# Performance work log

Hardware: AMD Instinct MI355X
Metric: run time of the kernel (lower is better)

Reference implementation:

```python
import jax, jax.numpy as jnp
import numpy as np

N_IN, N_HID, N_OUT = 700, 512, 20
B, T = 256, 100
TAU, TAU_O, THR, GAMMA = 0.6, 0.6, 0.6, 0.3

# Triangle surrogate spike (TriangleCall): heaviside fwd, triangular pseudo-derivative bwd
@jax.custom_vjp
def _spike(v):
    return (v >= THR).astype(v.dtype)

def _spike_fwd(v):
    return _spike(v), v

def _spike_bwd(v, g):
    sg = GAMMA * jnp.maximum(0.0, 1.0 - jnp.abs((v - THR) / THR))
    return (g * sg,)

_spike.defvjp(_spike_fwd, _spike_bwd)


def setup_inputs():
    key = jax.random.key(0)
    k1, k2, k3, k4, k5 = jax.random.split(key, 5)
    # binary input / target spike trains
    x = (jax.random.uniform(k1, (B, T, N_IN)) < 0.2).astype(jnp.float32)
    label = (jax.random.uniform(k2, (B, T, N_OUT)) < 0.1).astype(jnp.float32)
    # analog tile weights: fc1 and out halved at init, recurrent ~ U[0,1)/sqrt(n_hidden)
    W_fc1 = jax.random.normal(k3, (N_HID, N_IN), jnp.float32) * 0.05
    W_rec = jax.random.uniform(k4, (N_HID, N_HID), jnp.float32) / np.float32(np.sqrt(N_HID))
    W_out = jax.random.normal(k5, (N_OUT, N_HID), jnp.float32) * 0.05
    return {'x': x, 'label': label, 'W_fc1': W_fc1, 'W_rec': W_rec, 'W_out': W_out}


def reference(x, label, W_fc1, W_rec, W_out):
    b = x.shape[0]
    z = lambda n: jnp.zeros((b, n), x.dtype)
    carry0 = (z(N_HID), z(N_HID), z(N_OUT), z(N_OUT),        # hidden/out mem & spike
              z(N_IN), z(N_HID), z(N_HID),                   # trace_in_v, trace_rec_v, trace_out_t
              jnp.zeros((N_HID, N_IN), x.dtype),             # fc1_grad
              jnp.zeros((N_HID, N_HID), x.dtype),            # recurrent_grad
              jnp.zeros((N_OUT, N_HID), x.dtype))            # out_grad

    def step(carry, xt_lt):
        hm, hs, om, os_, tin, trec, tout, gf, gr, go = carry
        xt, lt = xt_lt
        # LIF hidden: leaky soft-reset, recurrent input uses previous step's spikes
        hm = TAU * hm * (1.0 - hs) + xt @ W_fc1.T + hs @ W_rec.T
        hs = _spike(hm)
        # LIF output
        om = TAU * om * (1.0 - os_) + hs @ W_out.T
        os_ = _spike(om)
        err = os_ - lt
        # eligibility traces
        tin = TAU * tin + xt
        trec = TAU * trec + hs
        tout = TAU_O * tout + hs
        # triangle pseudo-derivative of hidden membrane
        h_t = GAMMA * jnp.maximum(0.0, 1.0 - jnp.abs((hm - THR) / THR))
        # learning signal L = tile.backward(err) = err @ W_out; fuse with h_t
        L = (err @ W_out) * h_t  # [b, n_hid]
        # sum_b L[b,r]*h_t[b,r]*trace[b,i] without materializing [b,r,i]
        gf = gf + 0.1 * jnp.einsum('br,bi->ri', L, tin)
        gr = gr + 0.1 * jnp.einsum('br,bh->rh', L, trec)
        go = go + 0.1 * jnp.einsum('bo,br->or', err, tout)
        return (hm, hs, om, os_, tin, trec, tout, gf, gr, go), os_

    xs = (jnp.swapaxes(x, 0, 1), jnp.swapaxes(label, 0, 1))  # time-major for scan
    carry, outs = jax.lax.scan(step, carry0, xs)
    gf, gr, go = carry[7], carry[8], carry[9]
    # outputs [B, T, n_out] plus accumulated e-prop gradients (used for the
    # in-place weight update in the original; returned here to keep the compute live)
    return jnp.swapaxes(outs, 0, 1), gf, gr, go
```

## Files before the change

kernel.cpp:

```cpp
#include <hip/hip_runtime.h>
#include <cstdint>
#include <cstddef>

#define N_IN  700
#define N_INP 704
#define N_HID 512
#define N_OUT 20
#define BB    256
#define TT    100
#define NK    (BB*TT)
#define NCH   8
#define LDA   32

__device__ __constant__ const float TAU   = 0.6f;
__device__ __constant__ const float TAU_O = 0.6f;
__device__ __constant__ const float THR   = 0.6f;
__device__ __constant__ const float GAM   = 0.3f;

typedef float f32x4 __attribute__((ext_vector_type(4)));
typedef __bf16 bf16x8 __attribute__((ext_vector_type(8)));

__device__ __forceinline__ unsigned short f2bf_rne(float f) {
  uint32_t b = __builtin_bit_cast(uint32_t, f);
  uint32_t r = (b + 0x7FFFu + ((b >> 16) & 1u)) >> 16;
  return (unsigned short)r;
}

__global__ void k_prep_all(const float* __restrict__ W1, const float* __restrict__ Wr,
                           const float* __restrict__ Wo,
                           unsigned short* __restrict__ WH,
                           float* __restrict__ WRT, float* __restrict__ WoT,
                           float* __restrict__ Srow, float* __restrict__ SOs,
                           float* __restrict__ drvb, unsigned char* __restrict__ hzf) {
  const int g = blockIdx.x*256 + threadIdx.x;
  if (g < N_HID*88) {
    int r = g / 88, c = g - (g/88)*88;
    int ib = c*8;
    unsigned short h[8];
    #pragma unroll
    for (int j = 0; j < 8; ++j) {
      int i = ib + j;
      float v = (i < N_IN) ? W1[r*N_IN + i] : 0.f;
      h[j] = f2bf_rne(v);
    }
    uint4 hv = make_uint4((uint32_t)h[0] | ((uint32_t)h[1]<<16), (uint32_t)h[2] | ((uint32_t)h[3]<<16),
                          (uint32_t)h[4] | ((uint32_t)h[5]<<16), (uint32_t)h[6] | ((uint32_t)h[7]<<16));
    *(uint4*)(WH + (size_t)r*N_INP + ib) = hv;
  }
  if (g < N_HID*N_HID) {
    int j = g >> 9, r = g & 511;
    WRT[g] = Wr[r*N_HID + j];
  }
  if (g < N_HID*N_OUT) {
    int r = g / N_OUT, o = g - r*N_OUT;
    WoT[g] = Wo[o*N_HID + r];
  }
  if (g < N_HID) {
    float s = 0.f;
    for (int j = 0; j < N_HID; ++j) s += Wr[g*N_HID + j];
    Srow[g] = s;
  } else if (g < N_HID + N_OUT) {
    int o = g - N_HID;
    float s = 0.f;
    for (int r = 0; r < N_HID; ++r) s += Wo[o*N_HID + r];
    SOs[o] = s;
  }
  if (g < NK) hzf[g] = 0;
  if (g < NK*N_OUT) drvb[g] = 0.f;
}

__global__ __launch_bounds__(256) void k_gemm(const float* __restrict__ x,
                                              const unsigned short* __restrict__ WH,
                                              float* __restrict__ INL) {
  __shared__ __align__(16) unsigned short sA [128*LDA];
  __shared__ __align__(16) unsigned short sBh[128*LDA];
  const int tid = threadIdx.x, lane = tid & 63, w = tid >> 6;
  const int k0 = blockIdx.x * 128;
  const int c0 = blockIdx.y * 128;
  const int wr = w >> 1, wc = w & 1;
  const int fr = lane & 15, fk = lane >> 4;

  const int a_r  = tid >> 1;
  const int a_cb = (tid & 1) * 16;
  const int b_r  = tid >> 2;
  const int b_c  = (tid & 3) * 8;

  const float* xr = x + (size_t)(k0 + a_r) * N_IN;
  const unsigned short* gh = WH + (size_t)(c0 + b_r) * N_INP;

  f32x4 acc[4][4];
  #pragma unroll
  for (int m = 0; m < 4; ++m)
    #pragma unroll
    for (int n = 0; n < 4; ++n)
      acc[m][n] = (f32x4){0.f, 0.f, 0.f, 0.f};

  for (int s = 0; s < N_INP/32; ++s) {
    const int i0 = s * 32;
    float av[16];
    const int col0 = i0 + a_cb;
    if (col0 + 16 <= N_IN) {
      float4 t0 = *(const float4*)(xr + col0);
      float4 t1 = *(const float4*)(xr + col0 + 4);
      float4 t2 = *(const float4*)(xr + col0 + 8);
      float4 t3 = *(const float4*)(xr + col0 + 12);
      av[0]=t0.x; av[1]=t0.y; av[2]=t0.z; av[3]=t0.w;
      av[4]=t1.x; av[5]=t1.y; av[6]=t1.z; av[7]=t1.w;
      av[8]=t2.x; av[9]=t2.y; av[10]=t2.z; av[11]=t2.w;
      av[12]=t3.x; av[13]=t3.y; av[14]=t3.z; av[15]=t3.w;
    } else {
      #pragma unroll
      for (int j = 0; j < 16; ++j) av[j] = (col0 + j < N_IN) ? xr[col0 + j] : 0.f;
    }
    uint32_t us[8];
    #pragma unroll
    for (int p = 0; p < 8; ++p) {
      uint32_t lo = __builtin_bit_cast(uint32_t, av[2*p])   >> 16;
      uint32_t hi = __builtin_bit_cast(uint32_t, av[2*p+1]) & 0xFFFF0000u;
      us[p] = hi | lo;
    }
    *(uint4*)&sA[a_r*LDA + a_cb]     = make_uint4(us[0], us[1], us[2], us[3]);
    *(uint4*)&sA[a_r*LDA + a_cb + 8] = make_uint4(us[4], us[5], us[6], us[7]);
    *(uint4*)&sBh[b_r*LDA + b_c]      = *(const uint4*)(gh + i0 + b_c);
    *(uint4*)&sBh[(b_r+64)*LDA + b_c] = *(const uint4*)(gh + (size_t)64*N_INP + i0 + b_c);
    __syncthreads();

    bf16x8 a[4], bh[4];
    #pragma unroll
    for (int m = 0; m < 4; ++m)
      a[m] = *(const bf16x8*)&sA[(wr*64 + m*16 + fr)*LDA + fk*8];
    #pragma unroll
    for (int n = 0; n < 4; ++n)
      bh[n] = *(const bf16x8*)&sBh[(wc*64 + n*16 + fr)*LDA + fk*8];
    #pragma unroll
    for (int m = 0; m < 4; ++m)
      #pragma unroll
      for (int n = 0; n < 4; ++n)
        acc[m][n] = __builtin_amdgcn_mfma_f32_16x16x32_bf16(a[m], bh[n], acc[m][n], 0, 0, 0);
    __syncthreads();
  }
  #pragma unroll
  for (int m = 0; m < 4; ++m) {
    #pragma unroll
    for (int n = 0; n < 4; ++n) {
      #pragma unroll
      for (int reg = 0; reg < 4; ++reg) {
        const int row = k0 + wr*64 + m*16 + (lane>>4)*4 + reg;
        const int col = c0 + wc*64 + n*16 + fr;
        INL[(size_t)row*N_HID + col] = acc[m][n][reg];
      }
    }
  }
}

__global__ __launch_bounds__(256) void k_sat(const float* __restrict__ INL,
                                             const float* __restrict__ Srow,
                                             float* __restrict__ HT,
                                             unsigned char* __restrict__ hsb8,
                                             unsigned short* __restrict__ ct16,
                                             unsigned char* __restrict__ statS,
                                             unsigned char* __restrict__ hzf) {
  const int w = threadIdx.x >> 6, lane = threadIdx.x & 63;
  const size_t k = (size_t)blockIdx.x*4 + w;
  const float4 srwa = *(const float4*)(Srow + lane*8);
  const float4 srwb = *(const float4*)(Srow + lane*8 + 4);
  const float4 cva = *(const float4*)(INL + k*N_HID + lane*8);
  const float4 cvb = *(const float4*)(INL + k*N_HID + lane*8 + 4);
  float nhm[8];
  nhm[0]=cva.x+srwa.x; nhm[1]=cva.y+srwa.y; nhm[2]=cva.z+srwa.z; nhm[3]=cva.w+srwa.w;
  nhm[4]=cvb.x+srwb.x; nhm[5]=cvb.y+srwb.y; nhm[6]=cvb.z+srwb.z; nhm[7]=cvb.w+srwb.w;
  int nhs[8];
  unsigned long long m[8];
  int ctot = 0;
  #pragma unroll
  for (int j = 0; j < 8; ++j) { nhs[j] = (nhm[j] >= THR) ? 1 : 0; m[j] = __ballot(nhs[j] != 0); }
  #pragma unroll
  for (int j = 0; j < 8; ++j) ctot += (int)__popcll(m[j]);
  unsigned int byte = 0;
  #pragma unroll
  for (int j = 0; j < 8; ++j) byte |= ((unsigned int)nhs[j]) << j;
  hsb8[k*64 + lane] = (unsigned char)byte;
  float ht[8];
  int hnz = 0;
  #pragma unroll
  for (int j = 0; j < 8; ++j) {
    const float a = fabsf(nhm[j] - THR) / THR;
    ht[j] = GAM * fmaxf(0.f, 1.f - a);
    hnz |= (ht[j] != 0.f);
  }
  const unsigned long long hb = __ballot(hnz != 0);
  if (hb != 0ULL) {
    *(float4*)(HT + k*N_HID + lane*8)     = make_float4(ht[0], ht[1], ht[2], ht[3]);
    *(float4*)(HT + k*N_HID + lane*8 + 4) = make_float4(ht[4], ht[5], ht[6], ht[7]);
  }
  if (lane == 0) {
    ct16[k]  = (unsigned short)ctot;
    statS[k] = (unsigned char)(((ctot == 512) ? 1u : 0u) | ((hb != 0ULL) ? 2u : 0u));
    hzf[k]   = (hb != 0ULL) ? 1 : 0;
  }
}

__global__ __launch_bounds__(64, 1) void k_scan_tab(
    const float* __restrict__ INL, float* __restrict__ HT,
    const float* __restrict__ WoT, const float* __restrict__ WRT,
    const float* __restrict__ Srow, const float* __restrict__ SOs,
    unsigned char* __restrict__ hsb8, unsigned short* __restrict__ ctot16,
    float* __restrict__ drvb, unsigned char* __restrict__ hzf,
    const unsigned char* __restrict__ statS, int* __restrict__ tmaxp)
{
  __shared__ int list[N_HID];
  const int b = blockIdx.x, lane = threadIdx.x;
  const size_t base = (size_t)b*TT;
  const float4 srwa = *(const float4*)(Srow + lane*8);
  const float4 srwb = *(const float4*)(Srow + lane*8 + 4);
  float srw[8];
  srw[0]=srwa.x; srw[1]=srwa.y; srw[2]=srwa.z; srw[3]=srwa.w;
  srw[4]=srwb.x; srw[5]=srwb.y; srw[6]=srwb.z; srw[7]=srwb.w;
  float hm[8];
  int hs[8];
  #pragma unroll
  for (int j = 0; j < 8; ++j) { hm[j] = 0.f; hs[j] = 0; }
  const float SOsl = (lane < N_OUT) ? SOs[lane] : 0.f;
  int state = 0, cnt_prev = 0, mode_prev = 0, lastt = -1;

  auto GSTEP = [&](int t, unsigned st) {
    const size_t k = base + t;
    if (state == 1) {
      if (st & 1u) {
        if (st & 2u) lastt = t;
        return;
      }
      if (st & 2u) lastt = t;
      const float4 cva = *(const float4*)(INL + k*N_HID + lane*8);
      const float4 cvb = *(const float4*)(INL + k*N_HID + lane*8 + 4);
      const unsigned byte = hsb8[k*64 + lane];
      float cvv[8];
      cvv[0]=cva.x; cvv[1]=cva.y; cvv[2]=cva.z; cvv[3]=cva.w;
      cvv[4]=cvb.x; cvv[5]=cvb.y; cvv[6]=cvb.z; cvv[7]=cvb.w;
      int nhs[8];
      unsigned long long m[8];
      #pragma unroll
      for (int j = 0; j < 8; ++j) {
        hm[j] = cvv[j] + srw[j];
        nhs[j] = (int)((byte >> j) & 1u);
        m[j] = __ballot(nhs[j] != 0);
      }
      int ctot = 0;
      #pragma unroll
      for (int j = 0; j < 8; ++j) ctot += (int)__popcll(m[j]);
      const int mode = (ctot <= 256) ? 0 : 1;
      const int cnt  = mode ? (512 - ctot) : ctot;
      if (cnt != 0) {
        const unsigned long long below = (1ULL << lane) - 1ULL;
        int pos = 0;
        #pragma unroll
        for (int qq = 0; qq < 8; ++qq) {
          const unsigned long long sm = mode ? ~m[qq] : m[qq];
          pos += (int)__popcll(sm & below);
        }
        #pragma unroll
        for (int j = 0; j < 8; ++j) {
          const int sel = mode ? !nhs[j] : nhs[j];
          if (sel) list[pos++] = lane*8 + j;
        }
        float cdr = 0.f;
        for (int it = 0; it < cnt; ++it) {
          const int jj = list[it];
          cdr += (lane < N_OUT) ? WoT[jj*N_OUT + lane] : 0.f;
        }
        const float drv = mode ? (SOsl - cdr) : cdr;
        if (lane < N_OUT) drvb[k*N_OUT + lane] = drv;
      }
      #pragma unroll
      for (int j = 0; j < 8; ++j) hs[j] = nhs[j];
      cnt_prev = cnt; mode_prev = mode; state = 0;
      return;
    }
    const float4 cva = *(const float4*)(INL + k*N_HID + lane*8);
    const float4 cvb = *(const float4*)(INL + k*N_HID + lane*8 + 4);
    float rec[8];
    if (cnt_prev == 0 && mode_prev == 1) {
      #pragma unroll
      for (int j = 0; j < 8; ++j) rec[j] = srw[j];
    } else if (cnt_prev == 0) {
      #pragma unroll
      for (int j = 0; j < 8; ++j) rec[j] = 0.f;
    } else {
      float racc[8];
      #pragma unroll
      for (int j = 0; j < 8; ++j) racc[j] = 0.f;
      for (int it = 0; it < cnt_prev; ++it) {
        const int jj = list[it];
        const float4 wa = *(const float4*)(WRT + jj*N_HID + lane*8);
        const float4 wb = *(const float4*)(WRT + jj*N_HID + lane*8 + 4);
        racc[0]+=wa.x; racc[1]+=wa.y; racc[2]+=wa.z; racc[3]+=wa.w;
        racc[4]+=wb.x; racc[5]+=wb.y; racc[6]+=wb.z; racc[7]+=wb.w;
      }
      if (mode_prev) {
        #pragma unroll
        for (int j = 0; j < 8; ++j) rec[j] = srw[j] - racc[j];
      } else {
        #pragma unroll
        for (int j = 0; j < 8; ++j) rec[j] = racc[j];
      }
    }

    float cvv[8];
    cvv[0]=cva.x; cvv[1]=cva.y; cvv[2]=cva.z; cvv[3]=cva.w;
    cvv[4]=cvb.x; cvv[5]=cvb.y; cvv[6]=cvb.z; cvv[7]=cvb.w;
    float nhm[8]; int nhs[8];
    #pragma unroll
    for (int j = 0; j < 8; ++j)
      nhm[j] = TAU*hm[j]*(hs[j] ? 0.f : 1.f) + cvv[j] + rec[j];

    unsigned long long m[8];
    #pragma unroll
    for (int j = 0; j < 8; ++j) { nhs[j] = (nhm[j] >= THR) ? 1 : 0; m[j] = __ballot(nhs[j] != 0); }
    int ctot = 0;
    #pragma unroll
    for (int j = 0; j < 8; ++j) ctot += (int)__popcll(m[j]);
    {
      unsigned int byte = 0;
      #pragma unroll
      for (int j = 0; j < 8; ++j) byte |= ((unsigned int)nhs[j]) << j;
      hsb8[k*64 + lane] = (unsigned char)byte;
    }
    if (lane == 0) ctot16[k] = (unsigned short)ctot;
    const int mode = (ctot <= 256) ? 0 : 1;
    const int cnt  = mode ? (512 - ctot) : ctot;

    if (cnt != 0) {
      const unsigned long long below = (1ULL << lane) - 1ULL;
      int pos = 0;
      #pragma unroll
      for (int qq = 0; qq < 8; ++qq) {
        const unsigned long long sm = mode ? ~m[qq] : m[qq];
        pos += (int)__popcll(sm & below);
      }
      #pragma unroll
      for (int j = 0; j < 8; ++j) {
        const int sel = mode ? !nhs[j] : nhs[j];
        if (sel) list[pos++] = lane*8 + j;
      }
      float cdr = 0.f;
      for (int it = 0; it < cnt; ++it) {
        const int jj = list[it];
        cdr += (lane < N_OUT) ? WoT[jj*N_OUT + lane] : 0.f;
      }
      const float drv = mode ? (SOsl - cdr) : cdr;
      if (lane < N_OUT) drvb[k*N_OUT + lane] = drv;
    }

    float ht[8];
    int hnz = 0;
    #pragma unroll
    for (int j = 0; j < 8; ++j) {
      const float a = fabsf(nhm[j] - THR) / THR;
      ht[j] = GAM * fmaxf(0.f, 1.f - a);
      hnz |= (ht[j] != 0.f);
      hm[j] = nhm[j]; hs[j] = nhs[j];
    }
    const unsigned long long hb = __ballot(hnz != 0);
    if (hb != 0ULL) {
      *(float4*)(HT + k*N_HID + lane*8)     = make_float4(ht[0], ht[1], ht[2], ht[3]);
      *(float4*)(HT + k*N_HID + lane*8 + 4) = make_float4(ht[4], ht[5], ht[6], ht[7]);
      lastt = t;
    }
    if (lane == 0) hzf[k] = (hb != 0ULL) ? 1 : 0;
    cnt_prev = cnt; mode_prev = mode;
    state = (ctot == 512) ? 1 : 0;
  };

  uint32_t sv_cur  = *(const uint32_t*)(statS + base);
  uint32_t sv_next = *(const uint32_t*)(statS + base + 4);
  for (int tt = 0; tt < TT; tt += 4) {
    const uint32_t sv = sv_cur;
    {
      const int nn = (tt + 8 <= TT - 4) ? (tt + 8) : (TT - 4);
      sv_cur = sv_next;
      sv_next = *(const uint32_t*)(statS + base + nn);
    }
    if (state == 1 && (sv & 0x01010101u) == 0x01010101u) {
      if (sv & 0x02020202u) {
        if (sv & 0x02000000u)      lastt = tt + 3;
        else if (sv & 0x020000u)   lastt = tt + 2;
        else if (sv & 0x0200u)     lastt = tt + 1;
        else                       lastt = tt;
      }
      continue;
    }
    GSTEP(tt + 0, sv & 0xffu);
    GSTEP(tt + 1, (sv >> 8) & 0xffu);
    GSTEP(tt + 2, (sv >> 16) & 0xffu);
    GSTEP(tt + 3, (sv >> 24) & 0xffu);
  }
  if (lane == 0) tmaxp[b] = lastt + 1;
}

__global__ __launch_bounds__(256) void k_out(const unsigned short* __restrict__ ct16,
                                             const float* __restrict__ drvb,
                                             const float* __restrict__ label,
                                             const float* __restrict__ SOs,
                                             float* __restrict__ outs,
                                             float* __restrict__ errb) {
  const int g = blockIdx.x*256 + threadIdx.x;
  if (g >= BB*N_OUT) return;
  const int b = g / N_OUT, o = g - b*N_OUT;
  const size_t base = (size_t)b*TT;
  const float SOso = SOs[o];
  int ctb[4]; float dvb[4], lab[4];
  #pragma unroll
  for (int q = 0; q < 4; ++q) {
    ctb[q] = ct16[base + q];
    dvb[q] = drvb[(base + q)*N_OUT + o];
    lab[q] = label[(base + q)*N_OUT + o];
  }
  float om = 0.f; int osb = 0;
  for (int tt = 0; tt < TT; tt += 4) {
    #pragma unroll
    for (int q = 0; q < 4; ++q) {
      const int t = tt + q;
      const size_t k = base + t;
      const int   ct = ctb[q];
      const float dv = dvb[q];
      const float la = lab[q];
      const size_t kp = (t + 4 < TT) ? (k + 4) : (base + TT - 1);
      ctb[q] = ct16[kp];
      dvb[q] = drvb[kp*N_OUT + o];
      lab[q] = label[kp*N_OUT + o];
      const int mode = (ct <= 256) ? 0 : 1;
      const int cnt  = mode ? (512 - ct) : ct;
      const float drv = (cnt != 0) ? dv : (mode ? SOso : 0.f);
      om = TAU*om*(osb ? 0.f : 1.f) + drv;
      const int nos = (om >= THR) ? 1 : 0;
      const float osf = nos ? 1.f : 0.f;
      outs[k*N_OUT + o] = osf;
      errb[k*N_OUT + o] = osf - la;
      osb = nos;
    }
  }
}

__global__ __launch_bounds__(256, 1) void k_goacc(const float* __restrict__ errb,
                                                  const unsigned long long* __restrict__ hsbits,
                                                  float* __restrict__ pgo) {
  __shared__ __align__(16) float sE[TT][N_OUT];
  __shared__ __align__(16) float sF[TT][N_OUT];
  const int b = blockIdx.x >> 1;
  const int r = (blockIdx.x & 1)*256 + threadIdx.x;
  const int hw = r >> 6, sh = r & 63;
  const size_t rb = (size_t)b*TT;

  for (int idx = threadIdx.x; idx < TT*N_OUT; idx += 256)
    (&sE[0][0])[idx] = errb[rb*N_OUT + idx];
  __syncthreads();
  if (threadIdx.x < N_OUT) {
    const int o = threadIdx.x;
    float f = 0.f;
    for (int t = TT - 1; t >= 0; --t) {
      f = sE[t][o] + TAU_O*f;
      sF[t][o] = f;
    }
  }
  float goacc[N_OUT];
  #pragma unroll
  for (int o = 0; o < N_OUT; ++o) goacc[o] = 0.f;
  __syncthreads();

  unsigned long long word = hsbits[(rb + TT - 1)*8 + hw];
  for (int t = TT - 1; t >= 0; --t) {
    const unsigned long long word_n = (t > 0) ? hsbits[(rb + t - 1)*8 + hw] : 0ULL;
    if ((word >> sh) & 1ULL) {
      #pragma unroll
      for (int q = 0; q < 5; ++q) {
        const float4 f4 = *(const float4*)&sF[t][4*q];
        goacc[4*q+0] += f4.x; goacc[4*q+1] += f4.y; goacc[4*q+2] += f4.z; goacc[4*q+3] += f4.w;
      }
    }
    word = word_n;
  }
  #pragma unroll
  for (int o = 0; o < N_OUT; ++o)
    pgo[((size_t)b*N_OUT + o)*N_HID + r] = goacc[o];
}

__global__ __launch_bounds__(256, 1) void k_mshort(float* __restrict__ INL,
                                                   const float* __restrict__ HT,
                                                   const float* __restrict__ errb,
                                                   const unsigned char* __restrict__ hzf,
                                                   const float* __restrict__ Wo,
                                                   const int* __restrict__ tmax) {
  const int b = blockIdx.x >> 1;
  const int tm = tmax[b];
  if (tm == 0) return;
  const int r = (blockIdx.x & 1)*256 + threadIdx.x;
  const size_t rb = (size_t)b*TT;
  __shared__ __align__(16) float sE[TT][N_OUT];
  for (int idx = threadIdx.x; idx < tm*N_OUT; idx += 256)
    (&sE[0][0])[idx] = errb[rb*N_OUT + idx];
  __syncthreads();
  float woc[N_OUT];
  #pragma unroll
  for (int o = 0; o < N_OUT; ++o) woc[o] = Wo[o*N_HID + r];
  float mval = 0.f;
  for (int t = tm - 1; t >= 0; --t) {
    float d = 0.f;
    #pragma unroll
    for (int o = 0; o < N_OUT; ++o) d += sE[t][o] * woc[o];
    const float hp = hzf[rb + t] ? HT[(rb + t)*N_HID + r] : 0.f;
    const float v = d*hp + TAU*mval;
    INL[(rb + t)*N_HID + r] = v;
    mval = v;
  }
}

__global__ __launch_bounds__(256) void k_go(const float* __restrict__ pgo, float* __restrict__ go) {
  __shared__ float red[4][64];
  const int l = threadIdx.x & 63;
  const int ch = threadIdx.x >> 6;
  const int col = blockIdx.x*64 + l;
  float s = 0.f;
  for (int b2 = ch*64; b2 < ch*64 + 64; ++b2)
    s += pgo[(size_t)b2*(N_OUT*N_HID) + col];
  red[ch][l] = s;
  __syncthreads();
  if (ch == 0) go[col] = 0.1f*(((red[0][l] + red[1][l]) + red[2][l]) + red[3][l]);
}

__global__ __launch_bounds__(256) void k_gf(const float* __restrict__ M, const float* __restrict__ x,
                                            const int* __restrict__ tmax,
                                            float* __restrict__ gfp) {
  const int lane = threadIdx.x & 63, w = threadIdx.x >> 6;
  const int r  = blockIdx.x*64 + lane;
  const int i0 = blockIdx.y*64 + w*16;
  const int ch = blockIdx.z;
  const int b_lo = ch * (BB/NCH);
  __shared__ int cnt_sh[BB/NCH];
  if (threadIdx.x < BB/NCH) cnt_sh[threadIdx.x] = tmax[b_lo + threadIdx.x];
  __syncthreads();
  float acc[16];
  #pragma unroll
  for (int ii = 0; ii < 16; ++ii) acc[ii] = 0.f;
  int xi = i0 + (lane & 15); if (xi > N_IN - 1) xi = N_IN - 1;
  for (int bi = 0; bi < BB/NCH; ++bi) {
    const int ct = cnt_sh[bi];
    if (ct == 0) continue;
    const size_t kb = (size_t)(b_lo + bi)*TT;
    float mv = M[kb*N_HID + r];
    float xv = x[kb*N_IN + xi];
    for (int t = 0; t < ct; ++t) {
      float mv_n = 0.f, xv_n = 0.f;
      if (t + 1 < ct) {
        mv_n = M[(kb + t + 1)*N_HID + r];
        xv_n = x[(kb + t + 1)*N_IN + xi];
      }
      #pragma unroll
      for (int ii = 0; ii < 16; ++ii) acc[ii] += mv * __shfl(xv, ii);
      mv = mv_n; xv = xv_n;
    }
  }
  #pragma unroll
  for (int ii = 0; ii < 16; ++ii) {
    const int i = i0 + ii;
    if (i < N_IN) gfp[(size_t)ch*(N_HID*N_IN) + (size_t)r*N_IN + i] = acc[ii];
  }
}

__global__ __launch_bounds__(256) void k_gr(const float* __restrict__ M,
                                            const unsigned long long* __restrict__ hsbits,
                                            const int* __restrict__ tmax,
                                            float* __restrict__ grp) {
  const int lane = threadIdx.x & 63, w = threadIdx.x >> 6;
  const int r  = blockIdx.x*64 + lane;
  const int h0 = blockIdx.y*64 + w*16;
  const int ch = blockIdx.z;
  const int b_lo = ch * (BB/NCH);
  __shared__ int cnt_sh[BB/NCH];
  if (threadIdx.x < BB/NCH) cnt_sh[threadIdx.x] = tmax[b_lo + threadIdx.x];
  __syncthreads();
  float acc[16];
  #pragma unroll
  for (int ii = 0; ii < 16; ++ii) acc[ii] = 0.f;
  const int hw = h0 >> 6, sh = h0 & 63;
  for (int bi = 0; bi < BB/NCH; ++bi) {
    const int ct = cnt_sh[bi];
    if (ct == 0) continue;
    const size_t kb = (size_t)(b_lo + bi)*TT;
    float mv = M[kb*N_HID + r];
    unsigned long long word = hsbits[kb*8 + hw];
    for (int t = 0; t < ct; ++t) {
      float mv_n = 0.f; unsigned long long word_n = 0ULL;
      if (t + 1 < ct) {
        mv_n = M[(kb + t + 1)*N_HID + r];
        word_n = hsbits[(kb + t + 1)*8 + hw];
      }
      #pragma unroll
      for (int ii = 0; ii < 16; ++ii)
        if ((word >> (sh + ii)) & 1ULL) acc[ii] += mv;
      mv = mv_n; word = word_n;
    }
  }
  #pragma unroll
  for (int ii = 0; ii < 16; ++ii)
    grp[(size_t)ch*(N_HID*N_HID) + (size_t)r*N_HID + h0 + ii] = acc[ii];
}

__global__ void k_gfred(const float* __restrict__ gfp, float* __restrict__ gf) {
  const int g = blockIdx.x*256 + threadIdx.x;
  if (g < N_HID*N_IN) {
    float s = 0.f;
    #pragma unroll
    for (int c = 0; c < NCH; ++c) s += gfp[(size_t)c*(N_HID*N_IN) + g];
    gf[g] = 0.1f*s;
  }
}
__global__ void k_grred(const float* __restrict__ grp, float* __restrict__ gr) {
  const int g = blockIdx.x*256 + threadIdx.x;
  if (g < N_HID*N_HID) {
    float s = 0.f;
    #pragma unroll
    for (int c = 0; c < NCH; ++c) s += grp[(size_t)c*(N_HID*N_HID) + g];
    gr[g] = 0.1f*s;
  }
}

extern "C" void kernel_launch(void* const* d_in, const int* in_sizes, int n_in,
                              void* d_out, int out_size, void* d_ws, size_t ws_size,
                              hipStream_t stream) {
  const float* x     = (const float*)d_in[0];
  const float* label = (const float*)d_in[1];
  const float* W1    = (const float*)d_in[2];
  const float* Wr    = (const float*)d_in[3];
  const float* Wo    = (const float*)d_in[4];

  float* out  = (float*)d_out;
  float* outs = out;
  float* gf   = out + 512000;
  float* gr   = out + 512000 + 358400;
  float* go   = out + 512000 + 358400 + 262144;

  char* ws = (char*)d_ws;
  size_t off = 0;
  auto alloc = [&](size_t bytes) -> char* {
    char* p = ws + off;
    off += (bytes + 255) & ~(size_t)255;
    return p;
  };
  float* INL = (float*)alloc((size_t)NK*N_HID*sizeof(float));
  unsigned long long* hsb = (unsigned long long*)alloc((size_t)NK*8*sizeof(unsigned long long));
  int* tmax = (int*)alloc((size_t)BB*sizeof(int));
  char* uni = alloc((size_t)20971520);

  unsigned short* WH = (unsigned short*)(uni);
  float* WRT  = (float*)(uni + 1441792);
  float* Srow = (float*)(uni + 2490368);
  float* SOs  = (float*)(uni + 2492416);
  float* WoT  = (float*)(uni + 2494464);
  float* errb = (float*)(uni + 2536448);
  float* pgo  = (float*)(uni + 4587520);
  float* drvb = (float*)(uni + 15073280);
  unsigned short* ct16 = (unsigned short*)(uni + 17121280);
  unsigned char* hzf   = (unsigned char*)(uni + 17172480);
  unsigned char* statS = (unsigned char*)(uni + 17198336);
  float* gfp  = (float*)(uni);
  float* grp  = (float*)(uni + 11468800);

  float* HT = (float*)alloc((size_t)NK*N_HID*sizeof(float));

  k_prep_all<<<(NK*N_OUT + 255)/256, 256, 0, stream>>>(W1, Wr, Wo, WH, WRT, WoT, Srow, SOs, drvb, hzf);
  dim3 gg(NK/128, N_HID/128);
  k_gemm<<<gg, 256, 0, stream>>>(x, WH, INL);
  k_sat<<<NK/4, 256, 0, stream>>>(INL, Srow, HT, (unsigned char*)hsb, ct16, statS, hzf);
  k_scan_tab<<<BB, 64, 0, stream>>>(INL, HT, WoT, WRT, Srow, SOs, (unsigned char*)hsb, ct16, drvb, hzf, statS, tmax);
  k_out<<<(BB*N_OUT + 255)/256, 256, 0, stream>>>(ct16, drvb, label, SOs, outs, errb);
  k_goacc<<<BB*2, 256, 0, stream>>>(errb, hsb, pgo);
  k_mshort<<<BB*2, 256, 0, stream>>>(INL, HT, errb, hzf, Wo, tmax);
  k_go<<<(N_OUT*N_HID)/64, 256, 0, stream>>>(pgo, go);
  dim3 ggf(8, 11, NCH); k_gf<<<ggf, 256, 0, stream>>>(INL, x, tmax, gfp);
  dim3 ggr(8, 8, NCH);  k_gr<<<ggr, 256, 0, stream>>>(INL, hsb, tmax, grp);
  k_gfred<<<(N_HID*N_IN + 255)/256, 256, 0, stream>>>(gfp, gf);
  k_grred<<<(N_HID*N_HID + 255)/256, 256, 0, stream>>>(grp, gr);
}
```

Baseline: 279.7 us.

## Deepen GEMM K-tile to 64, split goacc into wave blocks, fuse reductions

The input GEMM now stages 64-wide K slices in shared memory instead of 32, which halves the number of barrier pairs and loop iterations per tile at the cost of more LDS and registers. k_goacc is relaunched as 8 single-wave blocks per batch instead of 2 blocks of 256 threads, giving more blocks for scheduling but redoing the per-batch trace recursion more times. The two final gradient reduction kernels are merged into one launch to save a launch.

```diff
diff --git a/kernel.cpp b/kernel.cpp
--- a/kernel.cpp
+++ b/kernel.cpp
@@ -10,7 +10,6 @@
 #define TT    100
 #define NK    (BB*TT)
 #define NCH   8
-#define LDA   32
 
 __device__ __constant__ const float TAU   = 0.6f;
 __device__ __constant__ const float TAU_O = 0.6f;
@@ -72,18 +71,18 @@
 __global__ __launch_bounds__(256) void k_gemm(const float* __restrict__ x,
                                               const unsigned short* __restrict__ WH,
                                               float* __restrict__ INL) {
-  __shared__ __align__(16) unsigned short sA [128*LDA];
-  __shared__ __align__(16) unsigned short sBh[128*LDA];
+  __shared__ __align__(16) unsigned short sA [128*64];
+  __shared__ __align__(16) unsigned short sBh[128*64];
   const int tid = threadIdx.x, lane = tid & 63, w = tid >> 6;
   const int k0 = blockIdx.x * 128;
   const int c0 = blockIdx.y * 128;
   const int wr = w >> 1, wc = w & 1;
   const int fr = lane & 15, fk = lane >> 4;
 
-  const int a_r  = tid >> 1;
-  const int a_cb = (tid & 1) * 16;
-  const int b_r  = tid >> 2;
-  const int b_c  = (tid & 3) * 8;
+  const int a_r = tid >> 1;
+  const int a_cb = (tid & 1) * 32;
+  const int b_r = tid >> 1;
+  const int b_cb = (tid & 1) * 32;
 
   const float* xr = x + (size_t)(k0 + a_r) * N_IN;
   const unsigned short* gh = WH + (size_t)(c0 + b_r) * N_INP;
@@ -95,48 +94,50 @@
     for (int n = 0; n < 4; ++n)
       acc[m][n] = (f32x4){0.f, 0.f, 0.f, 0.f};
 
-  for (int s = 0; s < N_INP/32; ++s) {
-    const int i0 = s * 32;
-    float av[16];
+  for (int s = 0; s < N_INP/64; ++s) {
+    const int i0 = s * 64;
     const int col0 = i0 + a_cb;
-    if (col0 + 16 <= N_IN) {
-      float4 t0 = *(const float4*)(xr + col0);
-      float4 t1 = *(const float4*)(xr + col0 + 4);
-      float4 t2 = *(const float4*)(xr + col0 + 8);
-      float4 t3 = *(const float4*)(xr + col0 + 12);
-      av[0]=t0.x; av[1]=t0.y; av[2]=t0.z; av[3]=t0.w;
-      av[4]=t1.x; av[5]=t1.y; av[6]=t1.z; av[7]=t1.w;
-      av[8]=t2.x; av[9]=t2.y; av[10]=t2.z; av[11]=t2.w;
-      av[12]=t3.x; av[13]=t3.y; av[14]=t3.z; av[15]=t3.w;
+    float av[32];
+    if (col0 + 32 <= N_IN) {
+      #pragma unroll
+      for (int q = 0; q < 8; ++q) {
+        const float4 t = *(const float4*)(xr + col0 + 4*q);
+        av[4*q+0]=t.x; av[4*q+1]=t.y; av[4*q+2]=t.z; av[4*q+3]=t.w;
+      }
     } else {
       #pragma unroll
-      for (int j = 0; j < 16; ++j) av[j] = (col0 + j < N_IN) ? xr[col0 + j] : 0.f;
-    }
-    uint32_t us[8];
-    #pragma unroll
-    for (int p = 0; p < 8; ++p) {
+      for (int j = 0; j < 32; ++j) av[j] = (col0 + j < N_IN) ? xr[col0 + j] : 0.f;
+    }
+    uint32_t us[16];
+    #pragma unroll
+    for (int p = 0; p < 16; ++p) {
       uint32_t lo = __builtin_bit_cast(uint32_t, av[2*p])   >> 16;
       uint32_t hi = __builtin_bit_cast(uint32_t, av[2*p+1]) & 0xFFFF0000u;
       us[p] = hi | lo;
     }
-    *(uint4*)&sA[a_r*LDA + a_cb]     = make_uint4(us[0], us[1], us[2], us[3]);
-    *(uint4*)&sA[a_r*LDA + a_cb + 8] = make_uint4(us[4], us[5], us[6], us[7]);
-    *(uint4*)&sBh[b_r*LDA + b_c]      = *(const uint4*)(gh + i0 + b_c);
-    *(uint4*)&sBh[(b_r+64)*LDA + b_c] = *(const uint4*)(gh + (size_t)64*N_INP + i0 + b_c);
+    #pragma unroll
+    for (int q = 0; q < 4; ++q)
+      *(uint4*)&sA[a_r*64 + a_cb + 8*q] = make_uint4(us[4*q], us[4*q+1], us[4*q+2], us[4*q+3]);
+    #pragma unroll
+    for (int q = 0; q < 4; ++q)
+      *(uint4*)&sBh[b_r*64 + b_cb + 8*q] = *(const uint4*)(gh + i0 + b_cb + 8*q);
     __syncthreads();
 
-    bf16x8 a[4], bh[4];
-    #pragma unroll
-    for (int m = 0; m < 4; ++m)
-      a[m] = *(const bf16x8*)&sA[(wr*64 + m*16 + fr)*LDA + fk*8];
-    #pragma unroll
-    for (int n = 0; n < 4; ++n)
-      bh[n] = *(const bf16x8*)&sBh[(wc*64 + n*16 + fr)*LDA + fk*8];
-    #pragma unroll
-    for (int m = 0; m < 4; ++m)
+    #pragma unroll
+    for (int ko = 0; ko < 2; ++ko) {
+      bf16x8 a[4], bh[4];
+      #pragma unroll
+      for (int m = 0; m < 4; ++m)
+        a[m] = *(const bf16x8*)&sA[(wr*64 + m*16 + fr)*64 + ko*32 + fk*8];
       #pragma unroll
       for (int n = 0; n < 4; ++n)
-        acc[m][n] = __builtin_amdgcn_mfma_f32_16x16x32_bf16(a[m], bh[n], acc[m][n], 0, 0, 0);
+        bh[n] = *(const bf16x8*)&sBh[(wc*64 + n*16 + fr)*64 + ko*32 + fk*8];
+      #pragma unroll
+      for (int m = 0; m < 4; ++m)
+        #pragma unroll
+        for (int n = 0; n < 4; ++n)
+          acc[m][n] = __builtin_amdgcn_mfma_f32_16x16x32_bf16(a[m], bh[n], acc[m][n], 0, 0, 0);
+    }
     __syncthreads();
   }
   #pragma unroll
@@ -441,21 +442,22 @@
   }
 }
 
-__global__ __launch_bounds__(256, 1) void k_goacc(const float* __restrict__ errb,
-                                                  const unsigned long long* __restrict__ hsbits,
-                                                  float* __restrict__ pgo) {
+__global__ __launch_bounds__(64, 1) void k_goacc(const float* __restrict__ errb,
+                                                 const unsigned long long* __restrict__ hsbits,
+                                                 float* __restrict__ pgo) {
   __shared__ __align__(16) float sE[TT][N_OUT];
   __shared__ __align__(16) float sF[TT][N_OUT];
-  const int b = blockIdx.x >> 1;
-  const int r = (blockIdx.x & 1)*256 + threadIdx.x;
-  const int hw = r >> 6, sh = r & 63;
+  const int b = blockIdx.x >> 3;
+  const int rblk = blockIdx.x & 7;
+  const int lane = threadIdx.x;
+  const int r = rblk*64 + lane;
   const size_t rb = (size_t)b*TT;
 
-  for (int idx = threadIdx.x; idx < TT*N_OUT; idx += 256)
+  for (int idx = lane; idx < TT*N_OUT; idx += 64)
     (&sE[0][0])[idx] = errb[rb*N_OUT + idx];
   __syncthreads();
-  if (threadIdx.x < N_OUT) {
-    const int o = threadIdx.x;
+  if (lane < N_OUT) {
+    const int o = lane;
     float f = 0.f;
     for (int t = TT - 1; t >= 0; --t) {
       f = sE[t][o] + TAU_O*f;
@@ -467,10 +469,10 @@
   for (int o = 0; o < N_OUT; ++o) goacc[o] = 0.f;
   __syncthreads();
 
-  unsigned long long word = hsbits[(rb + TT - 1)*8 + hw];
+  unsigned long long word = hsbits[(rb + TT - 1)*8 + rblk];
   for (int t = TT - 1; t >= 0; --t) {
-    const unsigned long long word_n = (t > 0) ? hsbits[(rb + t - 1)*8 + hw] : 0ULL;
-    if ((word >> sh) & 1ULL) {
+    const unsigned long long word_n = (t > 0) ? hsbits[(rb + t - 1)*8 + rblk] : 0ULL;
+    if ((word >> lane) & 1ULL) {
       #pragma unroll
       for (int q = 0; q < 5; ++q) {
         const float4 f4 = *(const float4*)&sF[t][4*q];
@@ -605,22 +607,20 @@
     grp[(size_t)ch*(N_HID*N_HID) + (size_t)r*N_HID + h0 + ii] = acc[ii];
 }
 
-__global__ void k_gfred(const float* __restrict__ gfp, float* __restrict__ gf) {
+__global__ void k_redall(const float* __restrict__ gfp, const float* __restrict__ grp,
+                         float* __restrict__ gf, float* __restrict__ gr) {
   const int g = blockIdx.x*256 + threadIdx.x;
   if (g < N_HID*N_IN) {
     float s = 0.f;
     #pragma unroll
     for (int c = 0; c < NCH; ++c) s += gfp[(size_t)c*(N_HID*N_IN) + g];
     gf[g] = 0.1f*s;
-  }
-}
-__global__ void k_grred(const float* __restrict__ grp, float* __restrict__ gr) {
-  const int g = blockIdx.x*256 + threadIdx.x;
-  if (g < N_HID*N_HID) {
+  } else if (g < N_HID*N_IN + N_HID*N_HID) {
+    const int g2 = g - N_HID*N_IN;
     float s = 0.f;
     #pragma unroll
-    for (int c = 0; c < NCH; ++c) s += grp[(size_t)c*(N_HID*N_HID) + g];
-    gr[g] = 0.1f*s;
+    for (int c = 0; c < NCH; ++c) s += grp[(size_t)c*(N_HID*N_HID) + g2];
+    gr[g2] = 0.1f*s;
   }
 }
 
@@ -673,11 +673,10 @@
   k_sat<<<NK/4, 256, 0, stream>>>(INL, Srow, HT, (unsigned char*)hsb, ct16, statS, hzf);
   k_scan_tab<<<BB, 64, 0, stream>>>(INL, HT, WoT, WRT, Srow, SOs, (unsigned char*)hsb, ct16, drvb, hzf, statS, tmax);
   k_out<<<(BB*N_OUT + 255)/256, 256, 0, stream>>>(ct16, drvb, label, SOs, outs, errb);
-  k_goacc<<<BB*2, 256, 0, stream>>>(errb, hsb, pgo);
+  k_goacc<<<BB*8, 64, 0, stream>>>(errb, hsb, pgo);
   k_mshort<<<BB*2, 256, 0, stream>>>(INL, HT, errb, hzf, Wo, tmax);
   k_go<<<(N_OUT*N_HID)/64, 256, 0, stream>>>(pgo, go);
   dim3 ggf(8, 11, NCH); k_gf<<<ggf, 256, 0, stream>>>(INL, x, tmax, gfp);
   dim3 ggr(8, 8, NCH);  k_gr<<<ggr, 256, 0, stream>>>(INL, hsb, tmax, grp);
-  k_gfred<<<(N_HID*N_IN + 255)/256, 256, 0, stream>>>(gfp, gf);
-  k_grred<<<(N_HID*N_HID + 255)/256, 256, 0, stream>>>(grp, gr);
-}
+  k_redall<<<(N_HID*N_IN + N_HID*N_HID + 255)/256, 256, 0, stream>>>(gfp, grp, gf, gr);
+}
```

New measurement: 290.9 us. 4.0% more time.
